# Performance work log

Hardware: AMD Instinct MI355X
Metric: run time of the kernel (lower is better)

Reference implementation:

```python
import jax, jax.numpy as jnp
import numpy as np

V, E, H, K = 50000, 256, 256, 16   # vocab, embed_dim, bi_lstm_hidden, n_tags (E must equal H)
HD = H // 2                        # per-direction hidden
B, NSEG, S = 32, 8, 128            # batch, segments, segment size
T = NSEG * S


def _lstm_dir(x, mask, Wih, Whh, b, h0, c0, reverse):
    """Masked (packed-equivalent) unidirectional LSTM. x:[T,B,E], mask:[T,B]."""
    def step(carry, inp):
        h, c = carry
        xt, mt = inp
        g = xt @ Wih.T + h @ Whh.T + b
        i, f, gg, o = jnp.split(g, 4, axis=-1)  # torch gate order i,f,g,o
        cn = jax.nn.sigmoid(f) * c + jax.nn.sigmoid(i) * jnp.tanh(gg)
        hn = jax.nn.sigmoid(o) * jnp.tanh(cn)
        m = mt[:, None]
        return (jnp.where(m, hn, h), jnp.where(m, cn, c)), jnp.where(m, hn, 0.0)
    (hT, cT), out = jax.lax.scan(step, (h0, c0), (x, mask), reverse=reverse)
    return out, (hT, cT)


def _bilstm(x, lengths, pf, pb, init=None):
    """pack_padded_sequence-equivalent BiLSTM. x:[T,B,E], lengths:[B]."""
    Tt, Bb = x.shape[0], x.shape[1]
    mask = jnp.arange(Tt)[:, None] < lengths[None, :]
    z = jnp.zeros((Bb, HD), x.dtype)
    h0f, c0f, h0b, c0b = init if init is not None else (z, z, z, z)
    of, (hf, cf) = _lstm_dir(x, mask, pf[0], pf[1], pf[2], h0f, c0f, False)
    ob, (hb, cb) = _lstm_dir(x, mask, pb[0], pb[1], pb[2], h0b, c0b, True)
    return jnp.concatenate([of, ob], -1), (hf, cf, hb, cb)


def _viterbi(emission, mask, start, trans, end):
    """torchcrf-style masked Viterbi decode. emission:[T,B,K], mask:[T,B]."""
    score = start[None, :] + emission[0]  # [B,K]
    def step(sc, inp):
        em, m = inp
        allsc = sc[:, :, None] + trans[None, :, :] + em[:, None, :]  # [B,K,K]
        best = jnp.max(allsc, axis=1)
        idx = jnp.argmax(allsc, axis=1).astype(jnp.int32)
        return jnp.where(m[:, None], best, sc), idx
    final, hist = jax.lax.scan(step, score, (emission[1:], mask[1:]))
    final = final + end[None, :]
    best_score = jnp.max(final, axis=-1)                 # [B]
    last = jnp.argmax(final, axis=-1).astype(jnp.int32)  # [B]
    def back(cur, inp):
        h, m = inp  # h:[B,K] backpointers at step t, m = mask[t+1]
        prev = jnp.take_along_axis(h, cur[:, None], axis=1)[:, 0]
        cur = jnp.where(m, prev, cur)
        return cur, cur
    _, tags_rev = jax.lax.scan(back, last, (hist, mask[1:]), reverse=True)
    tags = jnp.concatenate([tags_rev, last[None]], axis=0)  # [T,B]
    return tags, best_score


def _forward(texts, lengths, emb_table, Wih_f, Whh_f, bih_f, bhh_f,
             Wih_b, Whh_b, bih_b, bhh_b, Wlin, blin,
             crf_start, crf_trans, crf_end):
    pf = (Wih_f, Whh_f, bih_f + bhh_f)
    pb = (Wih_b, Whh_b, bih_b + bhh_b)
    emb = emb_table[texts]                      # [B,NSEG,S,E]
    x = jnp.transpose(emb, (1, 2, 0, 3))        # [NSEG,S,B,E]
    lens_seg = lengths.T                        # [NSEG,B]
    # pass 1: independent BiLSTM per segment (zero init state)
    outs, hids = jax.vmap(lambda xs, ls: _bilstm(xs, ls, pf, pb))(x, lens_seg)
    # positions >= per-segment max length are the raw embeddings (torch.cat with pad_text)
    maxlen = jnp.max(lens_seg, axis=1)          # [NSEG]
    over = jnp.arange(S)[None, :, None] >= maxlen[:, None, None]  # [NSEG,S,1]
    outs = jnp.where(over[..., None], x, outs)  # relies on E == 2*HD == H
    lstm1 = outs.reshape(NSEG * S, B, H)        # torch.cat(outputs, dim=0) -> [T,B,H]
    # get_text_lengths: per sample, valid tokens of all segments first, then pad tokens
    t_idx = jnp.arange(T)
    seg, pos = t_idx // S, t_idx % S
    valid = pos[None, :] < lengths[:, seg]                 # [B,T]
    key2 = jnp.where(valid, t_idx[None, :], t_idx[None, :] + T)
    perm = jnp.argsort(key2, axis=1)                       # [B,T] stable reorder
    lstm1_bt = jnp.transpose(lstm1, (1, 0, 2))             # [B,T,H]
    lstm2_in = jnp.transpose(
        jnp.take_along_axis(lstm1_bt, perm[..., None], axis=1), (1, 0, 2))  # [T,B,H]
    new_len = jnp.sum(lengths, axis=1)                     # [B]
    # pass 2: same LSTM weights, init state = final hidden of LAST segment (self.hidden)
    hf, cf, hb, cb = hids
    init = (hf[-1], cf[-1], hb[-1], cb[-1])
    lstm2_out, _ = _bilstm(lstm2_in, new_len, pf, pb, init)
    emission = lstm2_out @ Wlin.T + blin[None, None, :]    # [T,B,K]
    mask = jnp.arange(T)[:, None] < new_len[None, :]       # [T,B]
    return _viterbi(emission, mask, crf_start, crf_trans, crf_end)


def setup_inputs() -> dict:
    key = jax.random.key(0)
    ks = jax.random.split(key, 16)
    def u(k, shape, n):
        s = 1.0 / np.sqrt(n)
        return jax.random.uniform(k, shape, jnp.float32, -s, s)
    return {
        "texts": jax.random.randint(ks[0], (B, NSEG, S), 0, V).astype(jnp.int32),
        "lengths": jax.random.randint(ks[1], (B, NSEG), 1, S + 1).astype(jnp.int32),
        "emb_table": jax.random.normal(ks[2], (V, E), jnp.float32),
        "Wih_f": u(ks[3], (4 * HD, E), HD), "Whh_f": u(ks[4], (4 * HD, HD), HD),
        "bih_f": u(ks[5], (4 * HD,), HD), "bhh_f": u(ks[6], (4 * HD,), HD),
        "Wih_b": u(ks[7], (4 * HD, E), HD), "Whh_b": u(ks[8], (4 * HD, HD), HD),
        "bih_b": u(ks[9], (4 * HD,), HD), "bhh_b": u(ks[10], (4 * HD,), HD),
        "Wlin": u(ks[11], (K, H), H), "blin": u(ks[12], (K,), H),
        "crf_start": jax.random.uniform(ks[13], (K,), jnp.float32, -0.1, 0.1),
        "crf_trans": jax.random.uniform(ks[14], (K, K), jnp.float32, -0.1, 0.1),
        "crf_end": jax.random.uniform(ks[15], (K,), jnp.float32, -0.1, 0.1),
    }


def reference(texts, lengths, emb_table, Wih_f, Whh_f, bih_f, bhh_f,
              Wih_b, Whh_b, bih_b, bhh_b, Wlin, blin,
              crf_start, crf_trans, crf_end):
    # returns (tags [T,B] int32 padded with last tag beyond each length, viterbi score [B])
    return _forward(texts, lengths, emb_table, Wih_f, Whh_f, bih_f, bhh_f,
                    Wih_b, Whh_b, bih_b, bhh_b, Wlin, blin,
                    crf_start, crf_trans, crf_end)
```

## Files before the change

### kernel.cpp

```cpp
#include <hip/hip_runtime.h>
#include <cstdint>
#include <cstddef>


#define B_    32
#define NSEG_ 8
#define S_    128
#define T_    1024
#define E_    256
#define HD_   128
#define G_    512
#define K_    16
#define KS_   8

#define PIN4(v) asm volatile("" : "+v"((v).x), "+v"((v).y), "+v"((v).z), "+v"((v).w))

__device__ __forceinline__ float4 gload4(const float* p) {
    float4 d;
    asm volatile("global_load_dwordx4 %0, %1, off"
                 : "=v"(d) : "v"((unsigned long long)(uintptr_t)p));
    return d;
}
__device__ __forceinline__ void gstore1(float* p, float v) {
    asm volatile("global_store_dword %0, %1, off"
                 :: "v"((unsigned long long)(uintptr_t)p), "v"(v));
}

__global__ void prep_kernel(const int* __restrict__ lengths,
                            int* __restrict__ seg_off, int* __restrict__ new_len,
                            const float* __restrict__ bih_f, const float* __restrict__ bhh_f,
                            const float* __restrict__ bih_b, const float* __restrict__ bhh_b,
                            float* __restrict__ bias1,
                            const float* __restrict__ Wih_f, const float* __restrict__ Wih_b,
                            float* __restrict__ WT1)
{
    int gtid = blockIdx.x * blockDim.x + threadIdx.x;
    if (gtid < B_) {
        int acc = 0;
        for (int s = 0; s < NSEG_; s++) { seg_off[gtid*NSEG_ + s] = acc; acc += lengths[gtid*NSEG_ + s]; }
        new_len[gtid] = acc;
    }
    if (gtid < 1024) {
        int dir = gtid >> 9, w = gtid & 511, j = w >> 2, g = w & 3;
        int r = g * HD_ + j;
        bias1[gtid] = dir ? (bih_b[r] + bhh_b[r]) : (bih_f[r] + bhh_f[r]);
    }
    for (int e = gtid; e < 256*1024; e += gridDim.x * blockDim.x) {
        int k = e >> 10, jcol = e & 1023;
        int dir = jcol >> 9, w = jcol & 511, j = w >> 2, g = w & 3;
        int r = g * HD_ + j;
        WT1[e] = dir ? Wih_b[(size_t)r*E_ + k] : Wih_f[(size_t)r*E_ + k];
    }
}

template <int MODE>
__global__ void __launch_bounds__(256, 4)
proj_kernel(const int* __restrict__ texts, const float* __restrict__ emb,
            const float* __restrict__ WT1, const float* __restrict__ bias1,
            const float* __restrict__ lstm_packed, float* __restrict__ xproj,
            const int* __restrict__ seg_off, const int* __restrict__ new_len)
{
    int b  = blockIdx.z;
    int nl = new_len[b];
    int p0 = blockIdx.x * 32;
    if (p0 >= nl) return;
    int j0 = blockIdx.y * 256;

    __shared__ __align__(16) float As[32][256];
    __shared__ const float* rowp[32];
    int tid = threadIdx.x;
    if (tid < 32) {
        int p = p0 + tid;
        const float* r = emb;
        if (p < nl) {
            if (MODE == 0) {
                int sg = 0;
                #pragma unroll
                for (int q = 1; q < NSEG_; q++) if (seg_off[b*NSEG_ + q] <= p) sg = q;
                int t   = p - seg_off[b*NSEG_ + sg];
                int tok = texts[(b*NSEG_ + sg)*S_ + t];
                r = emb + (size_t)tok * E_;
            } else {
                r = lstm_packed + ((size_t)b*T_ + p) * 256;
            }
        }
        rowp[tid] = r;
    }
    __syncthreads();
    #pragma unroll 4
    for (int i = 0; i < 32; i++) As[i][tid] = rowp[i][tid];
    __syncthreads();

    int pg = tid >> 6;
    int jg = tid & 63;
    int j  = j0 + jg*4;
    float acc[8][4];
    #pragma unroll
    for (int i = 0; i < 8; i++) { acc[i][0]=0.f; acc[i][1]=0.f; acc[i][2]=0.f; acc[i][3]=0.f; }

    const float* wbase = WT1 + j;
    for (int k = 0; k < 256; k += 4) {
        float4 w0 = *(const float4*)(wbase + (size_t)(k+0)*1024);
        float4 w1 = *(const float4*)(wbase + (size_t)(k+1)*1024);
        float4 w2 = *(const float4*)(wbase + (size_t)(k+2)*1024);
        float4 w3 = *(const float4*)(wbase + (size_t)(k+3)*1024);
        #pragma unroll
        for (int i = 0; i < 8; i++) {
            float4 a = *(const float4*)&As[pg*8 + i][k];
            acc[i][0] = fmaf(a.w, w3.x, fmaf(a.z, w2.x, fmaf(a.y, w1.x, fmaf(a.x, w0.x, acc[i][0]))));
            acc[i][1] = fmaf(a.w, w3.y, fmaf(a.z, w2.y, fmaf(a.y, w1.y, fmaf(a.x, w0.y, acc[i][1]))));
            acc[i][2] = fmaf(a.w, w3.z, fmaf(a.z, w2.z, fmaf(a.y, w1.z, fmaf(a.x, w0.z, acc[i][2]))));
            acc[i][3] = fmaf(a.w, w3.w, fmaf(a.z, w2.w, fmaf(a.y, w1.w, fmaf(a.x, w0.w, acc[i][3]))));
        }
    }
    float4 bs = *(const float4*)(bias1 + j);
    #pragma unroll
    for (int i = 0; i < 8; i++) {
        int p = p0 + pg*8 + i;
        if (p < nl) {
            float4 r;
            r.x = acc[i][0] + bs.x; r.y = acc[i][1] + bs.y;
            r.z = acc[i][2] + bs.z; r.w = acc[i][3] + bs.w;
            *(float4*)(xproj + (((size_t)b*T_ + p) << 10) + j) = r;
        }
    }
}

__device__ __forceinline__ float sig_f(float x) { return 1.0f / (1.0f + __expf(-x)); }
__device__ __forceinline__ float tanh_f(float x) {
    float xc = fminf(fmaxf(x, -15.0f), 15.0f);
    float e  = __expf(-2.0f * xc);
    return (1.0f - e) / (1.0f + e);
}

__device__ __forceinline__ void lstm_chain(
    const float* __restrict__ Whh,
    const float* __restrict__ xp,
    float* __restrict__ outp,
    int p_base, int len, int dir, int rev,
    const float* __restrict__ h0, const float* __restrict__ c0,
    float* __restrict__ hT, float* __restrict__ cT)
{
    __shared__ __align__(16) float  h_sh[HD_];
    __shared__ __align__(16) float4 psum[4*HD_];
    int t = threadIdx.x;
    int j = t & 127, q = t >> 7;

    float4 w[4][8];
    #pragma unroll
    for (int g = 0; g < 4; g++) {
        const float4* wr = (const float4*)(Whh + (size_t)(j + 128*g) * HD_ + 32*q);
        #pragma unroll
        for (int i = 0; i < 8; i++) { w[g][i] = wr[i]; PIN4(w[g][i]); }
    }

    float c_reg = 0.0f;
    if (t < HD_) {
        h_sh[t] = h0 ? h0[t] : 0.0f;
        c_reg   = c0 ? c0[t] : 0.0f;
    }
    __syncthreads();

    const float* xbase = xp + dir * G_ + 4 * j;
    float*       obase = outp + dir * HD_ + j;

    float4 xc[KS_], xn[KS_];

    if (t < HD_ && len > 0) {
        #pragma unroll
        for (int u = 0; u < KS_; u++) {
            int s = u < len ? u : len - 1;
            int p = p_base + (rev ? (len - 1 - s) : s);
            xn[u] = gload4(xbase + ((size_t)p << 10));
        }
    }
    asm volatile("s_waitcnt vmcnt(0)");

    for (int gs = 0; gs < len; gs += KS_) {
        if (t < HD_) {
            #pragma unroll
            for (int u = 0; u < KS_; u++) { PIN4(xn[u]); xc[u] = xn[u]; }
            if (gs + KS_ < len) {
                #pragma unroll
                for (int u = 0; u < KS_; u++) {
                    int s = gs + KS_ + u; s = s < len ? s : len - 1;
                    int p = p_base + (rev ? (len - 1 - s) : s);
                    xn[u] = gload4(xbase + ((size_t)p << 10));
                }
            }
        }
        #pragma unroll
        for (int u = 0; u < KS_; u++) {
            if (gs + u < len) {
                const float4* hv = (const float4*)h_sh + q * 8;
                float4 a0 = make_float4(0.f,0.f,0.f,0.f);
                float4 a1 = a0, a2 = a0, a3 = a0;
                #pragma unroll
                for (int i = 0; i < 8; i++) {
                    float4 h4 = hv[i];
                    a0.x = fmaf(h4.x, w[0][i].x, a0.x); a0.y = fmaf(h4.y, w[0][i].y, a0.y);
                    a0.z = fmaf(h4.z, w[0][i].z, a0.z); a0.w = fmaf(h4.w, w[0][i].w, a0.w);
                    a1.x = fmaf(h4.x, w[1][i].x, a1.x); a1.y = fmaf(h4.y, w[1][i].y, a1.y);
                    a1.z = fmaf(h4.z, w[1][i].z, a1.z); a1.w = fmaf(h4.w, w[1][i].w, a1.w);
                    a2.x = fmaf(h4.x, w[2][i].x, a2.x); a2.y = fmaf(h4.y, w[2][i].y, a2.y);
                    a2.z = fmaf(h4.z, w[2][i].z, a2.z); a2.w = fmaf(h4.w, w[2][i].w, a2.w);
                    a3.x = fmaf(h4.x, w[3][i].x, a3.x); a3.y = fmaf(h4.y, w[3][i].y, a3.y);
                    a3.z = fmaf(h4.z, w[3][i].z, a3.z); a3.w = fmaf(h4.w, w[3][i].w, a3.w);
                }
                psum[q*128 + j] = make_float4((a0.x+a0.y)+(a0.z+a0.w),
                                              (a1.x+a1.y)+(a1.z+a1.w),
                                              (a2.x+a2.y)+(a2.z+a2.w),
                                              (a3.x+a3.y)+(a3.z+a3.w));
                __syncthreads();
                if (t < HD_) {
                    float4 p0 = psum[j], p1 = psum[128 + j], p2 = psum[256 + j], p3 = psum[384 + j];
                    float gi = xc[u].x + ((p0.x + p1.x) + (p2.x + p3.x));
                    float gf = xc[u].y + ((p0.y + p1.y) + (p2.y + p3.y));
                    float gg = xc[u].z + ((p0.z + p1.z) + (p2.z + p3.z));
                    float go = xc[u].w + ((p0.w + p1.w) + (p2.w + p3.w));
                    float cn = sig_f(gf) * c_reg + sig_f(gi) * tanh_f(gg);
                    c_reg = cn;
                    float hn = sig_f(go) * tanh_f(cn);
                    h_sh[j] = hn;
                    int s = gs + u;
                    int p = p_base + (rev ? (len - 1 - s) : s);
                    gstore1(obase + (size_t)p * 256, hn);
                }
                __syncthreads();
            }
        }
        asm volatile("s_waitcnt vmcnt(8)");
    }
    if (hT != nullptr && t < HD_) { hT[t] = h_sh[t]; cT[t] = c_reg; }
    asm volatile("s_waitcnt vmcnt(0)");
}

__global__ void __launch_bounds__(512, 2)
lstm1_kernel(const int* __restrict__ lengths, const int* __restrict__ seg_off,
             const float* __restrict__ Whh_f, const float* __restrict__ Whh_b,
             const float* __restrict__ xproj, float* __restrict__ lstm_packed,
             float* __restrict__ hinit, float* __restrict__ cinit)
{
    int cid = blockIdx.x;
    int b = cid >> 4, seg = (cid >> 1) & 7, dir = cid & 1;
    int len = lengths[b*NSEG_ + seg];
    int pb  = seg_off[b*NSEG_ + seg];
    const float* Whh = dir ? Whh_b : Whh_f;
    float* hT = nullptr; float* cT = nullptr;
    if (seg == NSEG_ - 1) {
        hT = hinit + (dir*B_ + b)*HD_;
        cT = cinit + (dir*B_ + b)*HD_;
    }
    lstm_chain(Whh, xproj + ((size_t)b << 20), lstm_packed + (size_t)b*T_*256,
               pb, len, dir, dir, nullptr, nullptr, hT, cT);
}

__global__ void __launch_bounds__(512, 2)
lstm2_kernel(const int* __restrict__ new_len,
             const float* __restrict__ Whh_f, const float* __restrict__ Whh_b,
             const float* __restrict__ xproj, float* __restrict__ lstm_packed,
             const float* __restrict__ hinit, const float* __restrict__ cinit)
{
    int cid = blockIdx.x;
    int b = cid >> 1, dir = cid & 1;
    int len = new_len[b];
    const float* Whh = dir ? Whh_b : Whh_f;
    lstm_chain(Whh, xproj + ((size_t)b << 20), lstm_packed + (size_t)b*T_*256,
               0, len, dir, dir,
               hinit + (dir*B_ + b)*HD_, cinit + (dir*B_ + b)*HD_,
               nullptr, nullptr);
}

__global__ void __launch_bounds__(256)
emission_kernel(const float* __restrict__ lstm_packed, const float* __restrict__ Wlin,
                const float* __restrict__ blin, float* __restrict__ emis,
                const int* __restrict__ new_len)
{
    int b  = blockIdx.y;
    int nl = new_len[b];
    int p0 = blockIdx.x * 16;
    if (p0 >= nl) return;
    int pl = threadIdx.x >> 4, s = threadIdx.x & 15;
    int p  = p0 + pl;
    const float4* xr = (const float4*)(lstm_packed + ((size_t)b*T_ + p) * 256);
    const float4* wr = (const float4*)(Wlin + (size_t)s * 256);
    float ax = 0.f, ay = 0.f, az = 0.f, aw = 0.f;
    #pragma unroll
    for (int i = 0; i < 64; i++) {
        float4 a = xr[i]; float4 ww = wr[i];
        ax = fmaf(a.x, ww.x, ax); ay = fmaf(a.y, ww.y, ay);
        az = fmaf(a.z, ww.z, az); aw = fmaf(a.w, ww.w, aw);
    }
    if (p < nl) emis[((size_t)b*T_ + p)*K_ + s] = (ax + ay) + (az + aw) + blin[s];
}

__global__ void __launch_bounds__(64)
viterbi_kernel(const float* __restrict__ emis, const float* __restrict__ start,
               const float* __restrict__ trans, const float* __restrict__ endv,
               const int* __restrict__ new_len, float* __restrict__ out)
{
    int b    = blockIdx.x;
    int nl   = new_len[b];
    int lane = threadIdx.x;
    int s    = lane & 15, q4 = lane >> 4;

    __shared__ unsigned char hist[T_ * K_];
    __shared__ unsigned char tagb[T_];

    float tr[4];
    #pragma unroll
    for (int jj = 0; jj < 4; jj++) tr[jj] = trans[(q4*4 + jj)*K_ + s];

    const float* em = emis + (size_t)b * T_ * K_;
    float sc = start[s] + em[s];

    for (int p = 1; p < nl; p++) {
        float e = em[p*K_ + s];
        float m = -3.4e38f; int a = 0;
        #pragma unroll
        for (int jj = 0; jj < 4; jj++) {
            int q   = q4*4 + jj;
            float sq = __shfl(sc, q, 16);
            float v  = sq + tr[jj];
            if (v > m) { m = v; a = q; }
        }
        #pragma unroll
        for (int d = 16; d < 64; d <<= 1) {
            float mo = __shfl_xor(m, d);
            int   ao = __shfl_xor(a, d);
            if (mo > m || (mo == m && ao < a)) { m = mo; a = ao; }
        }
        sc = m + e;
        if (lane < K_) hist[p*K_ + s] = (unsigned char)a;
    }

    float m = sc + endv[s]; int a = s;
    #pragma unroll
    for (int d = 1; d < 16; d <<= 1) {
        float mo = __shfl_xor(m, d);
        int   ao = __shfl_xor(a, d);
        if (mo > m || (mo == m && ao < a)) { m = mo; a = ao; }
    }
    int last = a;
    if (lane == 0) out[T_*B_ + b] = m;
    __syncthreads();

    for (int i = lane; i < T_; i += 64) tagb[i] = (unsigned char)last;
    __syncthreads();
    if (lane == 0) {
        int cur = last;
        for (int j = nl - 2; j >= 0; j--) {
            cur = hist[(j+1)*K_ + cur];
            tagb[j] = (unsigned char)cur;
        }
    }
    __syncthreads();
    for (int i = lane; i < T_; i += 64) out[(size_t)i*B_ + b] = (float)tagb[i];
}

extern "C" void kernel_launch(void* const* d_in, const int* in_sizes, int n_in,
                              void* d_out, int out_size, void* d_ws, size_t ws_size,
                              hipStream_t stream)
{
    (void)in_sizes; (void)n_in; (void)out_size; (void)ws_size;
    const int*   texts   = (const int*)  d_in[0];
    const int*   lengths = (const int*)  d_in[1];
    const float* emb     = (const float*)d_in[2];
    const float* Wih_f   = (const float*)d_in[3];
    const float* Whh_f   = (const float*)d_in[4];
    const float* bih_f   = (const float*)d_in[5];
    const float* bhh_f   = (const float*)d_in[6];
    const float* Wih_b   = (const float*)d_in[7];
    const float* Whh_b   = (const float*)d_in[8];
    const float* bih_b   = (const float*)d_in[9];
    const float* bhh_b   = (const float*)d_in[10];
    const float* Wlin    = (const float*)d_in[11];
    const float* blin    = (const float*)d_in[12];
    const float* c_start = (const float*)d_in[13];
    const float* c_trans = (const float*)d_in[14];
    const float* c_end   = (const float*)d_in[15];
    float* out = (float*)d_out;

    char* w = (char*)d_ws;
    int*   seg_off     = (int*)(w);
    int*   new_len     = (int*)(w + 1024);
    float* bias1       = (float*)(w + 4096);
    float* WT1         = (float*)(w + 8192);
    float* hinit       = (float*)(w + 8192 + 1048576);
    float* cinit       = hinit + 8192;
    float* lstm_packed = cinit + 8192;
    float* xproj       = lstm_packed + (size_t)B_*T_*256;
    float* emis        = xproj + ((size_t)B_ << 20);

    prep_kernel<<<128, 256, 0, stream>>>(lengths, seg_off, new_len,
                                         bih_f, bhh_f, bih_b, bhh_b, bias1,
                                         Wih_f, Wih_b, WT1);
    proj_kernel<0><<<dim3(32, 4, B_), 256, 0, stream>>>(texts, emb, WT1, bias1,
                                                        lstm_packed, xproj, seg_off, new_len);
    lstm1_kernel<<<512, 512, 0, stream>>>(lengths, seg_off, Whh_f, Whh_b,
                                          xproj, lstm_packed, hinit, cinit);
    proj_kernel<1><<<dim3(32, 4, B_), 256, 0, stream>>>(texts, emb, WT1, bias1,
                                                        lstm_packed, xproj, seg_off, new_len);
    lstm2_kernel<<<64, 512, 0, stream>>>(new_len, Whh_f, Whh_b,
                                         xproj, lstm_packed, hinit, cinit);
    emission_kernel<<<dim3(64, B_), 256, 0, stream>>>(lstm_packed, Wlin, blin, emis, new_len);
    viterbi_kernel<<<B_, 64, 0, stream>>>(emis, c_start, c_trans, c_end, new_len, out);
}
```

Measured before the change: 1.624 ms.

## Distribute LSTM cell update across all waves with one barrier per step

Restructures the recurrent LSTM step so every wave redundantly computes the gate nonlinearities for its own 32-hidden slice. Each lane pair sums half of the partials and combines them with a shuffle. Double-buffered psum and per-wave h staging remove the second __syncthreads per timestep. Output stores are batched per 8-step group and written late from registers, and the inline-asm loads and stores plus manual waitcnt are replaced with plain C++ accesses. The cost is redundant transcendental work on every wave and more register pressure from hbuf.

```diff
diff --git a/kernel.cpp b/kernel.cpp
--- a/kernel.cpp
+++ b/kernel.cpp
@@ -14,17 +14,6 @@
 #define KS_   8
 
 #define PIN4(v) asm volatile("" : "+v"((v).x), "+v"((v).y), "+v"((v).z), "+v"((v).w))
-
-__device__ __forceinline__ float4 gload4(const float* p) {
-    float4 d;
-    asm volatile("global_load_dwordx4 %0, %1, off"
-                 : "=v"(d) : "v"((unsigned long long)(uintptr_t)p));
-    return d;
-}
-__device__ __forceinline__ void gstore1(float* p, float v) {
-    asm volatile("global_store_dword %0, %1, off"
-                 :: "v"((unsigned long long)(uintptr_t)p), "v"(v));
-}
 
 __global__ void prep_kernel(const int* __restrict__ lengths,
                             int* __restrict__ seg_off, int* __restrict__ new_len,
@@ -141,98 +130,116 @@
     const float* __restrict__ h0, const float* __restrict__ c0,
     float* __restrict__ hT, float* __restrict__ cT)
 {
-    __shared__ __align__(16) float  h_sh[HD_];
-    __shared__ __align__(16) float4 psum[4*HD_];
+    __shared__ __align__(16) float  h_stage[8*32];
+    __shared__ __align__(16) float4 psum[2*4*HD_];
+
     int t = threadIdx.x;
-    int j = t & 127, q = t >> 7;
-
-    float4 w[4][8];
+    int w = t >> 6, L = t & 63;
+    int q = w >> 1;
+    int jF = t & 127;
+    int jj = 32*q + (L >> 1);
+    int half = L & 1;
+    bool storer = ((w & 1) == 0) && ((L & 1) == 0);
+
+    float4 wgt[4][8];
     #pragma unroll
     for (int g = 0; g < 4; g++) {
-        const float4* wr = (const float4*)(Whh + (size_t)(j + 128*g) * HD_ + 32*q);
-        #pragma unroll
-        for (int i = 0; i < 8; i++) { w[g][i] = wr[i]; PIN4(w[g][i]); }
-    }
-
-    float c_reg = 0.0f;
-    if (t < HD_) {
-        h_sh[t] = h0 ? h0[t] : 0.0f;
-        c_reg   = c0 ? c0[t] : 0.0f;
-    }
-    __syncthreads();
-
-    const float* xbase = xp + dir * G_ + 4 * j;
-    float*       obase = outp + dir * HD_ + j;
+        const float4* wr = (const float4*)(Whh + (size_t)(jF + 128*g) * HD_ + 32*q);
+        #pragma unroll
+        for (int i = 0; i < 8; i++) { wgt[g][i] = wr[i]; PIN4(wgt[g][i]); }
+    }
+
+    float c_reg = c0 ? c0[jj] : 0.0f;
+    if (L < 32) h_stage[32*w + L] = h0 ? h0[32*q + L] : 0.0f;
+    __syncthreads();
+
+    const float* xb = xp + dir * G_ + 4 * jj;
+    float*       ob = outp + dir * HD_ + jj;
 
     float4 xc[KS_], xn[KS_];
-
-    if (t < HD_ && len > 0) {
+    float  hbuf[KS_];
+
+    #pragma unroll
+    for (int u = 0; u < KS_; u++) {
+        int s = u < len ? u : (len - 1);
+        int p = p_base + (rev ? (len - 1 - s) : s);
+        xn[u] = *(const float4*)(xb + ((size_t)p << 10));
+    }
+
+    for (int gs = 0; gs < len; gs += KS_) {
+        if (storer && gs > 0) {
+            #pragma unroll
+            for (int u = 0; u < KS_; u++) {
+                int s = gs - KS_ + u;
+                int p = p_base + (rev ? (len - 1 - s) : s);
+                ob[(size_t)p * 256] = hbuf[u];
+            }
+        }
+        #pragma unroll
+        for (int u = 0; u < KS_; u++) xc[u] = xn[u];
+        if (gs + KS_ < len) {
+            #pragma unroll
+            for (int u = 0; u < KS_; u++) {
+                int s = gs + KS_ + u; s = s < len ? s : (len - 1);
+                int p = p_base + (rev ? (len - 1 - s) : s);
+                xn[u] = *(const float4*)(xb + ((size_t)p << 10));
+            }
+        }
         #pragma unroll
         for (int u = 0; u < KS_; u++) {
-            int s = u < len ? u : len - 1;
-            int p = p_base + (rev ? (len - 1 - s) : s);
-            xn[u] = gload4(xbase + ((size_t)p << 10));
-        }
-    }
-    asm volatile("s_waitcnt vmcnt(0)");
-
-    for (int gs = 0; gs < len; gs += KS_) {
-        if (t < HD_) {
-            #pragma unroll
-            for (int u = 0; u < KS_; u++) { PIN4(xn[u]); xc[u] = xn[u]; }
-            if (gs + KS_ < len) {
-                #pragma unroll
-                for (int u = 0; u < KS_; u++) {
-                    int s = gs + KS_ + u; s = s < len ? s : len - 1;
-                    int p = p_base + (rev ? (len - 1 - s) : s);
-                    xn[u] = gload4(xbase + ((size_t)p << 10));
-                }
-            }
-        }
-        #pragma unroll
-        for (int u = 0; u < KS_; u++) {
-            if (gs + u < len) {
-                const float4* hv = (const float4*)h_sh + q * 8;
+            int sstep = gs + u;
+            if (sstep < len) {
+                int buf = (sstep & 1) * (4*HD_);
+                const float4* hv = (const float4*)(h_stage + 32*w);
                 float4 a0 = make_float4(0.f,0.f,0.f,0.f);
                 float4 a1 = a0, a2 = a0, a3 = a0;
                 #pragma unroll
                 for (int i = 0; i < 8; i++) {
                     float4 h4 = hv[i];
-                    a0.x = fmaf(h4.x, w[0][i].x, a0.x); a0.y = fmaf(h4.y, w[0][i].y, a0.y);
-                    a0.z = fmaf(h4.z, w[0][i].z, a0.z); a0.w = fmaf(h4.w, w[0][i].w, a0.w);
-                    a1.x = fmaf(h4.x, w[1][i].x, a1.x); a1.y = fmaf(h4.y, w[1][i].y, a1.y);
-                    a1.z = fmaf(h4.z, w[1][i].z, a1.z); a1.w = fmaf(h4.w, w[1][i].w, a1.w);
-                    a2.x = fmaf(h4.x, w[2][i].x, a2.x); a2.y = fmaf(h4.y, w[2][i].y, a2.y);
-                    a2.z = fmaf(h4.z, w[2][i].z, a2.z); a2.w = fmaf(h4.w, w[2][i].w, a2.w);
-                    a3.x = fmaf(h4.x, w[3][i].x, a3.x); a3.y = fmaf(h4.y, w[3][i].y, a3.y);
-                    a3.z = fmaf(h4.z, w[3][i].z, a3.z); a3.w = fmaf(h4.w, w[3][i].w, a3.w);
+                    a0.x = fmaf(h4.x, wgt[0][i].x, a0.x); a0.y = fmaf(h4.y, wgt[0][i].y, a0.y);
+                    a0.z = fmaf(h4.z, wgt[0][i].z, a0.z); a0.w = fmaf(h4.w, wgt[0][i].w, a0.w);
+                    a1.x = fmaf(h4.x, wgt[1][i].x, a1.x); a1.y = fmaf(h4.y, wgt[1][i].y, a1.y);
+                    a1.z = fmaf(h4.z, wgt[1][i].z, a1.z); a1.w = fmaf(h4.w, wgt[1][i].w, a1.w);
+                    a2.x = fmaf(h4.x, wgt[2][i].x, a2.x); a2.y = fmaf(h4.y, wgt[2][i].y, a2.y);
+                    a2.z = fmaf(h4.z, wgt[2][i].z, a2.z); a2.w = fmaf(h4.w, wgt[2][i].w, a2.w);
+                    a3.x = fmaf(h4.x, wgt[3][i].x, a3.x); a3.y = fmaf(h4.y, wgt[3][i].y, a3.y);
+                    a3.z = fmaf(h4.z, wgt[3][i].z, a3.z); a3.w = fmaf(h4.w, wgt[3][i].w, a3.w);
                 }
-                psum[q*128 + j] = make_float4((a0.x+a0.y)+(a0.z+a0.w),
-                                              (a1.x+a1.y)+(a1.z+a1.w),
-                                              (a2.x+a2.y)+(a2.z+a2.w),
-                                              (a3.x+a3.y)+(a3.z+a3.w));
+                psum[buf + q*HD_ + jF] = make_float4((a0.x+a0.y)+(a0.z+a0.w),
+                                                     (a1.x+a1.y)+(a1.z+a1.w),
+                                                     (a2.x+a2.y)+(a2.z+a2.w),
+                                                     (a3.x+a3.y)+(a3.z+a3.w));
                 __syncthreads();
-                if (t < HD_) {
-                    float4 p0 = psum[j], p1 = psum[128 + j], p2 = psum[256 + j], p3 = psum[384 + j];
-                    float gi = xc[u].x + ((p0.x + p1.x) + (p2.x + p3.x));
-                    float gf = xc[u].y + ((p0.y + p1.y) + (p2.y + p3.y));
-                    float gg = xc[u].z + ((p0.z + p1.z) + (p2.z + p3.z));
-                    float go = xc[u].w + ((p0.w + p1.w) + (p2.w + p3.w));
-                    float cn = sig_f(gf) * c_reg + sig_f(gi) * tanh_f(gg);
-                    c_reg = cn;
-                    float hn = sig_f(go) * tanh_f(cn);
-                    h_sh[j] = hn;
-                    int s = gs + u;
-                    int p = p_base + (rev ? (len - 1 - s) : s);
-                    gstore1(obase + (size_t)p * 256, hn);
+                float4 s0 = psum[buf + (2*half)*HD_ + jj];
+                float4 s1 = psum[buf + (2*half+1)*HD_ + jj];
+                float sx = s0.x + s1.x, sy = s0.y + s1.y;
+                float sz = s0.z + s1.z, sw = s0.w + s1.w;
+                float gi = xc[u].x + sx + __shfl_xor(sx, 1);
+                float gf = xc[u].y + sy + __shfl_xor(sy, 1);
+                float gg = xc[u].z + sz + __shfl_xor(sz, 1);
+                float go = xc[u].w + sw + __shfl_xor(sw, 1);
+                float cn = sig_f(gf) * c_reg + sig_f(gi) * tanh_f(gg);
+                c_reg = cn;
+                float hn = sig_f(go) * tanh_f(cn);
+                if (!(L & 1)) h_stage[32*w + (L >> 1)] = hn;
+                hbuf[u] = hn;
+                if (sstep == len - 1 && hT != nullptr && storer) {
+                    hT[jj] = hn; cT[jj] = c_reg;
                 }
-                __syncthreads();
             }
         }
-        asm volatile("s_waitcnt vmcnt(8)");
-    }
-    if (hT != nullptr && t < HD_) { hT[t] = h_sh[t]; cT[t] = c_reg; }
-    asm volatile("s_waitcnt vmcnt(0)");
+    }
+    if (storer && len > 0) {
+        int gs0 = ((len - 1) / KS_) * KS_;
+        #pragma unroll
+        for (int u = 0; u < KS_; u++) {
+            int s = gs0 + u;
+            if (s < len) {
+                int p = p_base + (rev ? (len - 1 - s) : s);
+                ob[(size_t)p * 256] = hbuf[u];
+            }
+        }
+    }
 }
 
 __global__ void __launch_bounds__(512, 2)
```

After: 1.804 ms. +11.1%, slower.
